# Kernel tuning notes

Hardware: AMD Instinct MI355X
Metric: run time of the kernel (lower is better)

The kernel has to match this reference:

```python
import jax, jax.numpy as jnp
import numpy as np

B, N, IN_DIM, HID = 8, 2048, 128, 64
LN_EPS = 1e-5
NEG_INF = -9e15
LRELU_SLOPE = 0.2


def setup_inputs() -> dict:
    key = jax.random.key(0)
    k1, k2, k3, k4, k5, k6 = jax.random.split(key, 6)
    stdv = 1.0 / np.sqrt(HID)
    adj = jax.random.randint(k1, (B, N, N), 0, 2, dtype=jnp.int32)
    # ensure self-loops so every row has at least one valid entry
    adj = adj.at[:, jnp.arange(N), jnp.arange(N)].set(1)
    return {
        "adj": adj,
        "x": jax.random.normal(k2, (B, N, IN_DIM), dtype=jnp.float32),
        "h": jax.random.normal(k3, (B, N, HID), dtype=jnp.float32),
        "X2H": jax.random.uniform(k4, (IN_DIM, 3 * HID), minval=-stdv, maxval=stdv, dtype=jnp.float32),
        "H2H": jax.random.uniform(k5, (HID, 3 * HID), minval=-stdv, maxval=stdv, dtype=jnp.float32),
        "a": jax.random.uniform(k6, (2 * HID, 1), minval=-stdv, maxval=stdv, dtype=jnp.float32),
    }


def _gated_inputs(x, h, X2H, H2H):
    gate_x = x @ X2H          # [B,N,3H]
    gate_h = h @ H2H          # [B,N,3H]
    i_r, i_i, i_n = jnp.split(gate_x, 3, axis=2)
    h_r, h_i, h_n = jnp.split(gate_h, 3, axis=2)
    resetgate = jax.nn.sigmoid(i_r + h_r)
    inputgate = jax.nn.sigmoid(i_i + h_i)
    irh = i_n + resetgate * h_n
    mu = jnp.mean(irh, axis=-1, keepdims=True)
    var = jnp.mean(jnp.square(irh - mu), axis=-1, keepdims=True)
    irh = (irh - mu) * jax.lax.rsqrt(var + LN_EPS)  # layer_norm, no affine
    newgate = jnp.tanh(irh)
    return newgate + inputgate * (h - newgate)


def reference(adj, x, h, X2H, H2H, a):
    Wh = _gated_inputs(x, h, X2H, H2H)              # [B,N,H]
    Wh1 = Wh @ a[:HID]                              # [B,N,1]
    Wh2 = Wh @ a[HID:]                              # [B,N,1]
    e = jax.nn.leaky_relu(Wh1 + jnp.swapaxes(Wh2, 1, 2), LRELU_SLOPE)  # [B,N,N]
    scores = jnp.where(adj != 0, e, jnp.float32(NEG_INF))
    attention = jax.nn.softmax(scores, axis=2)
    h_prime = attention @ Wh                        # [B,N,H]
    return (h_prime, Wh)
```

## Files before the change

### kernel.cpp

```cpp
#include <hip/hip_runtime.h>

constexpr int BB  = 8;
constexpr int NN  = 2048;
constexpr int IND = 128;
constexpr int HD  = 64;
constexpr float LN_EPS = 1e-5f;
constexpr float SLOPE  = 0.2f;

typedef _Float16 half8 __attribute__((ext_vector_type(8)));
typedef _Float16 half4 __attribute__((ext_vector_type(4)));
typedef float    f32x4 __attribute__((ext_vector_type(4)));

__device__ __forceinline__ float wave_sum(float v) {
    #pragma unroll
    for (int off = 32; off > 0; off >>= 1) v += __shfl_xor(v, off);
    return v;
}
__device__ __forceinline__ float wave_max(float v) {
    #pragma unroll
    for (int off = 32; off > 0; off >>= 1) v = fmaxf(v, __shfl_xor(v, off));
    return v;
}

__global__ void k_prep(const float* __restrict__ X2H, const float* __restrict__ H2H,
                       _Float16* __restrict__ Wt)
{
    const int tot = 256 * 192;
    for (int idx = blockIdx.x * 256 + threadIdx.x; idx < tot; idx += gridDim.x * 256) {
        const int col = idx / 192, k = idx % 192;
        float v;
        if (col < 128)       v = (k < 128) ? X2H[(size_t)k * 192 + col]
                                           : H2H[(size_t)(k - 128) * 192 + col];
        else if (col < 192)  v = (k < 128) ? X2H[(size_t)k * 192 + col] : 0.f;
        else                 v = (k >= 128) ? H2H[(size_t)(k - 128) * 192 + (col - 64)] : 0.f;
        Wt[idx] = (_Float16)v;
    }
}

__global__ __launch_bounds__(256, 4) void k_gates(
    const float* __restrict__ x, const float* __restrict__ h,
    const _Float16* __restrict__ Wt, const float* __restrict__ a,
    float* __restrict__ Wh_out, _Float16* __restrict__ Whh2,
    float* __restrict__ Wh1, float* __restrict__ Wh2)
{
    __shared__ float gbuf[16][260];

    const int tid = threadIdx.x, lane = tid & 63, w = tid >> 6;
    const int m = lane & 15, q = lane >> 4;
    const int row0 = blockIdx.x * 16;

    f32x4 acc[4];
    #pragma unroll
    for (int ct = 0; ct < 4; ++ct) acc[ct] = (f32x4){0.f, 0.f, 0.f, 0.f};

    #pragma unroll
    for (int kc = 0; kc < 6; ++kc) {
        half8 a8;
        if (kc < 4) {
            const float* xp = x + (size_t)(row0 + m) * IND + kc * 32 + q * 8;
            const f32x4 v0 = *(const f32x4*)xp;
            const f32x4 v1 = *(const f32x4*)(xp + 4);
            #pragma unroll
            for (int j = 0; j < 4; ++j) { a8[j] = (_Float16)v0[j]; a8[4 + j] = (_Float16)v1[j]; }
        } else {
            const float* hp_ = h + (size_t)(row0 + m) * HD + (kc - 4) * 32 + q * 8;
            const f32x4 v0 = *(const f32x4*)hp_;
            const f32x4 v1 = *(const f32x4*)(hp_ + 4);
            #pragma unroll
            for (int j = 0; j < 4; ++j) { a8[j] = (_Float16)v0[j]; a8[4 + j] = (_Float16)v1[j]; }
        }
        #pragma unroll
        for (int ct = 0; ct < 4; ++ct) {
            const half8 b8 = *(const half8*)(Wt + ((size_t)(w * 64 + ct * 16 + m) * 192 + kc * 32 + q * 8));
            acc[ct] = __builtin_amdgcn_mfma_f32_16x16x32_f16(a8, b8, acc[ct], 0, 0, 0);
        }
    }

    #pragma unroll
    for (int ct = 0; ct < 4; ++ct)
        #pragma unroll
        for (int r2 = 0; r2 < 4; ++r2)
            gbuf[q * 4 + r2][w * 64 + ct * 16 + m] = acc[ct][r2];
    __syncthreads();

    const float a0 = a[lane], a1 = a[64 + lane];
    half4 p4;
    const int grow0 = row0 + w * 4;
    #pragma unroll
    for (int r = 0; r < 4; ++r) {
        const int row = w * 4 + r;
        const int grow = row0 + row;
        const float g0 = gbuf[row][lane];
        const float g1 = gbuf[row][64 + lane];
        const float g2 = gbuf[row][128 + lane];
        const float g3 = gbuf[row][192 + lane];
        const float rg = 1.f / (1.f + __expf(-g0));
        const float ig = 1.f / (1.f + __expf(-g1));
        const float irh = g2 + rg * g3;
        const float mu = wave_sum(irh) * (1.f / 64.f);
        const float dv = irh - mu;
        const float var = wave_sum(dv * dv) * (1.f / 64.f);
        const float ng = tanhf(dv * rsqrtf(var + LN_EPS));
        const float hr = h[(size_t)grow * HD + lane];
        const float wh = ng + ig * (hr - ng);
        Wh_out[(size_t)grow * HD + lane] = wh;
        p4[r] = (_Float16)wh;
        const float d1 = wave_sum(wh * a0);
        const float d2 = wave_sum(wh * a1);
        if (lane == 0) { Wh1[grow] = d1; Wh2[grow] = d2; }
    }
    *(half4*)(Whh2 + ((size_t)(grow0 >> 3) * 64 + lane) * 8 + (w & 1) * 4) = p4;
}

constexpr int KC  = 256;
constexpr int PST = KC + 8;

__global__ __launch_bounds__(512, 4) void k_attn(
    const int* __restrict__ adj,
    const _Float16* __restrict__ Whh2,
    const float* __restrict__ Wh1, const float* __restrict__ Wh2,
    float* __restrict__ hp)
{
    __shared__ __align__(16) _Float16 Pall[8 * 16 * PST];
    __shared__ float ssum[8][16];
    __shared__ float redb[8];

    const int tid  = threadIdx.x;
    const int lane = tid & 63;
    const int w    = tid >> 6;
    const int b    = blockIdx.x >> 7;
    const int i0   = (blockIdx.x & 127) * 16;
    const int m    = lane & 15;
    const int q    = lane >> 4;

    _Float16* __restrict__ Pw = Pall + w * 16 * PST;

    const f32x4 wv = ((const f32x4*)(Wh2 + (size_t)b * NN))[w * 64 + lane];

    float mx = fmaxf(fmaxf(wv[0], wv[1]), fmaxf(wv[2], wv[3]));
    mx = wave_max(mx);
    if (lane == 0) redb[w] = mx;
    __syncthreads();
    float M = redb[0];
    #pragma unroll
    for (int i = 1; i < 8; ++i) M = fmaxf(M, redb[i]);

    float w1r[16];
    #pragma unroll
    for (int r = 0; r < 16; ++r) w1r[r] = Wh1[b * NN + i0 + r];

    const int* __restrict__ abase = adj + ((size_t)b * NN + i0) * NN + w * KC + 4 * lane;

    int4 buf0[4], buf1[4];
    #pragma unroll
    for (int r = 0; r < 4; ++r) buf0[r] = *(const int4*)(abase + (size_t)r * NN);
    #pragma unroll
    for (int r = 0; r < 4; ++r) buf1[r] = *(const int4*)(abase + (size_t)(4 + r) * NN);

    #pragma unroll
    for (int g = 0; g < 4; ++g) {
        #pragma unroll
        for (int rr = 0; rr < 4; ++rr) {
            const int r = g * 4 + rr;
            const int4 av = (g & 1) ? buf1[rr] : buf0[rr];
            const int ai[4] = {av.x, av.y, av.z, av.w};
            const float t0 = w1r[r] + M;
            const float c  = (t0 > 0.f) ? t0 : SLOPE * t0;
            half4 ph;
            float s = 0.f;
            #pragma unroll
            for (int d = 0; d < 4; ++d) {
                const float t = w1r[r] + wv[d];
                const float e = (t > 0.f) ? t : SLOPE * t;
                const float p = ai[d] ? __expf(e - c) : 0.f;
                s += p;
                ph[d] = (_Float16)p;
            }
            s = wave_sum(s);
            if (lane == 0) ssum[w][r] = s;
            *(half4*)&Pw[r * PST + 4 * lane] = ph;
        }
        if (g + 2 < 4) {
            #pragma unroll
            for (int rr = 0; rr < 4; ++rr) {
                int4 nv = *(const int4*)(abase + (size_t)((g + 2) * 4 + rr) * NN);
                if (g & 1) buf1[rr] = nv; else buf0[rr] = nv;
            }
        }
    }
    __syncthreads();

    const half8* __restrict__ Wp = (const half8*)(Whh2 + (size_t)b * NN * HD);
    f32x4 acc[4];
    #pragma unroll
    for (int cc = 0; cc < 4; ++cc) acc[cc] = (f32x4){0.f, 0.f, 0.f, 0.f};

    #pragma unroll
    for (int k8 = 0; k8 < 8; ++k8) {
        const half8 a8 = *(const half8*)&Pw[m * PST + k8 * 32 + q * 8];
        #pragma unroll
        for (int cc = 0; cc < 4; ++cc) {
            const half8 b8 = Wp[(size_t)(w * 32 + k8 * 4 + q) * 64 + cc * 16 + m];
            acc[cc] = __builtin_amdgcn_mfma_f32_16x16x32_f16(a8, b8, acc[cc], 0, 0, 0);
        }
    }
    __syncthreads();

    float* __restrict__ accb = (float*)Pall;
    #pragma unroll
    for (int cc = 0; cc < 4; ++cc)
        *(f32x4*)&accb[(w * 64 + lane) * 17 + cc * 4] = acc[cc];
    __syncthreads();

    if (w < 4) {
        f32x4 tot = (f32x4){0.f, 0.f, 0.f, 0.f};
        #pragma unroll
        for (int wp = 0; wp < 8; ++wp) {
            const f32x4 t4 = *(const f32x4*)&accb[(wp * 64 + lane) * 17 + w * 4];
            tot[0] += t4[0]; tot[1] += t4[1]; tot[2] += t4[2]; tot[3] += t4[3];
        }
        #pragma unroll
        for (int r2 = 0; r2 < 4; ++r2) {
            const int irow = q * 4 + r2;
            float S = 0.f;
            #pragma unroll
            for (int wp = 0; wp < 8; ++wp) S += ssum[wp][irow];
            hp[((size_t)b * NN + i0 + irow) * HD + w * 16 + m] = tot[r2] / S;
        }
    }
}

extern "C" void kernel_launch(void* const* d_in, const int* in_sizes, int n_in,
                              void* d_out, int out_size, void* d_ws, size_t ws_size,
                              hipStream_t stream) {
    const int*   adj = (const int*)d_in[0];
    const float* x   = (const float*)d_in[1];
    const float* h   = (const float*)d_in[2];
    const float* X2H = (const float*)d_in[3];
    const float* H2H = (const float*)d_in[4];
    const float* a   = (const float*)d_in[5];

    float* out = (float*)d_out;
    float* hp  = out;
    float* Wh  = out + (size_t)BB * NN * HD;

    float*    Wh1  = (float*)d_ws;
    float*    Wh2  = Wh1 + BB * NN;
    _Float16* Whh2 = (_Float16*)(Wh2 + BB * NN);
    _Float16* Wt   = Whh2 + (size_t)BB * NN * HD;

    k_prep<<<dim3(64), dim3(256), 0, stream>>>(X2H, H2H, Wt);
    k_gates<<<dim3((BB * NN) / 16), dim3(256), 0, stream>>>(
        x, h, Wt, a, Wh, Whh2, Wh1, Wh2);
    k_attn<<<dim3(BB * (NN / 16)), dim3(512), 0, stream>>>(
        adj, Whh2, Wh1, Wh2, hp);
}
```

Measured before the change: 239.3 us.

## Factor attention exp into rank-1 terms and compress adjacency into bitmasks

Splits the fused attention kernel into three stages. An aux kernel precomputes per-row and per-column exponential factors, using the fact that leaky-relu of a sum is one of two linear branches, so exp(e - c) factors as u_i*v_j or u'_i*v'_j. A score kernel streams the int32 adjacency once and packs it, together with the branch sign, into 2-bit-per-entry masks. The PV kernel rebuilds P on the fly in fp16 from these factors and computes the row sums with an extra MFMA against ones. This moves the adjacency read into a simple bandwidth-bound pass and removes per-element exp and the LDS round-trip for P. In exchange there are two extra launches, a mask buffer written and re-read, and a possible precision change because the probabilities are now formed as fp16 products.

```diff
diff --git a/kernel.cpp b/kernel.cpp
--- a/kernel.cpp
+++ b/kernel.cpp
@@ -112,122 +112,149 @@
     *(half4*)(Whh2 + ((size_t)(grow0 >> 3) * 64 + lane) * 8 + (w & 1) * 4) = p4;
 }
 
-constexpr int KC  = 256;
-constexpr int PST = KC + 8;
-
-__global__ __launch_bounds__(512, 4) void k_attn(
+__global__ __launch_bounds__(256) void k_aux(
+    const float* __restrict__ Wh1, const float* __restrict__ Wh2,
+    float* __restrict__ u, float* __restrict__ up,
+    _Float16* __restrict__ v16, _Float16* __restrict__ v16p)
+{
+    __shared__ float red[4];
+    const int tid = threadIdx.x, lane = tid & 63, w = tid >> 6;
+    const int b = blockIdx.x >> 3, part = blockIdx.x & 7;
+
+    float mx = -3e38f;
+    #pragma unroll
+    for (int k = 0; k < 8; ++k) mx = fmaxf(mx, Wh2[b * NN + k * 256 + tid]);
+    mx = wave_max(mx);
+    if (lane == 0) red[w] = mx;
+    __syncthreads();
+    const float M = fmaxf(fmaxf(red[0], red[1]), fmaxf(red[2], red[3]));
+
+    const int grow = b * NN + part * 256 + tid;
+    const float t0 = Wh1[grow] + M;
+    const float c  = (t0 > 0.f) ? t0 : SLOPE * t0;
+    u[grow]  = __expf(t0 - c);
+    up[grow] = __expf(SLOPE * t0 - c);
+    const float w2 = Wh2[grow] - M;
+    v16[grow]  = (_Float16)__expf(w2);
+    v16p[grow] = (_Float16)__expf(SLOPE * w2);
+}
+
+__global__ __launch_bounds__(256, 8) void k_score(
     const int* __restrict__ adj,
+    const float* __restrict__ Wh1, const float* __restrict__ Wh2,
+    unsigned short* __restrict__ Mb)
+{
+    const int tid = threadIdx.x;
+    const int4* __restrict__ adj4 = (const int4*)adj;
+
+    #pragma unroll
+    for (int s = 0; s < 4; ++s) {
+        const int row = s * 4096 + blockIdx.x;
+        const int b   = row >> 11;
+        const float negw1 = -Wh1[row];
+
+        const int4 a0 = adj4[(size_t)row * 512 + tid * 2];
+        const int4 a1 = adj4[(size_t)row * 512 + tid * 2 + 1];
+        const f32x4 w0 = ((const f32x4*)(Wh2 + (size_t)b * NN))[tid * 2];
+        const f32x4 w1 = ((const f32x4*)(Wh2 + (size_t)b * NN))[tid * 2 + 1];
+
+        unsigned m1 = 0, m0 = 0;
+        const int av[8] = {a0.x, a0.y, a0.z, a0.w, a1.x, a1.y, a1.z, a1.w};
+        #pragma unroll
+        for (int j = 0; j < 8; ++j) {
+            const float wj = (j < 4) ? w0[j] : w1[j - 4];
+            const bool a = (av[j] != 0);
+            const bool ss = (wj > negw1);
+            m1 |= (unsigned)(a && ss) << j;
+            m0 |= (unsigned)(a && !ss) << j;
+        }
+        Mb[(size_t)row * 256 + tid] = (unsigned short)(m1 | (m0 << 8));
+    }
+}
+
+__global__ __launch_bounds__(256, 4) void k_pv(
+    const unsigned short* __restrict__ Mb,
     const _Float16* __restrict__ Whh2,
-    const float* __restrict__ Wh1, const float* __restrict__ Wh2,
+    const _Float16* __restrict__ v16, const _Float16* __restrict__ v16p,
+    const float* __restrict__ u, const float* __restrict__ up,
     float* __restrict__ hp)
 {
-    __shared__ __align__(16) _Float16 Pall[8 * 16 * PST];
-    __shared__ float ssum[8][16];
-    __shared__ float redb[8];
-
-    const int tid  = threadIdx.x;
-    const int lane = tid & 63;
-    const int w    = tid >> 6;
-    const int b    = blockIdx.x >> 7;
-    const int i0   = (blockIdx.x & 127) * 16;
-    const int m    = lane & 15;
-    const int q    = lane >> 4;
-
-    _Float16* __restrict__ Pw = Pall + w * 16 * PST;
-
-    const f32x4 wv = ((const f32x4*)(Wh2 + (size_t)b * NN))[w * 64 + lane];
-
-    float mx = fmaxf(fmaxf(wv[0], wv[1]), fmaxf(wv[2], wv[3]));
-    mx = wave_max(mx);
-    if (lane == 0) redb[w] = mx;
+    __shared__ float accb[4][64][20];
+    __shared__ float ssumw[4][16];
+
+    const int tid = threadIdx.x, lane = tid & 63, w = tid >> 6;
+    const int m = lane & 15, q = lane >> 4;
+    const int b  = blockIdx.x >> 7;
+    const int i0 = (blockIdx.x & 127) * 16;
+
+    const int grow_m = b * NN + i0 + m;
+    const _Float16 uh  = (_Float16)u[grow_m];
+    const _Float16 uph = (_Float16)up[grow_m];
+
+    const unsigned short* __restrict__ mrow = Mb + (size_t)grow_m * 256 + w * 64;
+    const half8* __restrict__ Wp  = (const half8*)Whh2 + (size_t)b * 16384;
+    const half8* __restrict__ v8  = (const half8*)v16  + b * 256;
+    const half8* __restrict__ v8p = (const half8*)v16p + b * 256;
+
+    half8 ones;
+    #pragma unroll
+    for (int j = 0; j < 8; ++j) ones[j] = (_Float16)1.f;
+
+    f32x4 acc[4];
+    #pragma unroll
+    for (int cc = 0; cc < 4; ++cc) acc[cc] = (f32x4){0.f, 0.f, 0.f, 0.f};
+    f32x4 accS = (f32x4){0.f, 0.f, 0.f, 0.f};
+
+    #pragma unroll
+    for (int k8 = 0; k8 < 16; ++k8) {
+        const int slot  = k8 * 4 + q;
+        const int kpack = w * 64 + slot;
+        const unsigned mb = mrow[slot];
+        const unsigned m1b = mb & 0xFFu, m0b = mb >> 8;
+
+        const half8 vj  = v8[kpack];
+        const half8 vjp = v8p[kpack];
+
+        half8 Ac;
+        #pragma unroll
+        for (int j = 0; j < 8; ++j) {
+            const _Float16 pos = uh * vj[j];
+            const _Float16 neg = uph * vjp[j];
+            Ac[j] = (m1b >> j & 1u) ? pos : ((m0b >> j & 1u) ? neg : (_Float16)0.f);
+        }
+
+        accS = __builtin_amdgcn_mfma_f32_16x16x32_f16(Ac, ones, accS, 0, 0, 0);
+        #pragma unroll
+        for (int cc = 0; cc < 4; ++cc) {
+            const half8 b8 = Wp[(size_t)kpack * 64 + cc * 16 + m];
+            acc[cc] = __builtin_amdgcn_mfma_f32_16x16x32_f16(Ac, b8, acc[cc], 0, 0, 0);
+        }
+    }
+
+    if (m == 0) {
+        #pragma unroll
+        for (int r2 = 0; r2 < 4; ++r2) ssumw[w][q * 4 + r2] = accS[r2];
+    }
+    #pragma unroll
+    for (int cc = 0; cc < 4; ++cc)
+        *(f32x4*)&accb[w][lane][cc * 4] = acc[cc];
     __syncthreads();
-    float M = redb[0];
-    #pragma unroll
-    for (int i = 1; i < 8; ++i) M = fmaxf(M, redb[i]);
-
-    float w1r[16];
-    #pragma unroll
-    for (int r = 0; r < 16; ++r) w1r[r] = Wh1[b * NN + i0 + r];
-
-    const int* __restrict__ abase = adj + ((size_t)b * NN + i0) * NN + w * KC + 4 * lane;
-
-    int4 buf0[4], buf1[4];
-    #pragma unroll
-    for (int r = 0; r < 4; ++r) buf0[r] = *(const int4*)(abase + (size_t)r * NN);
-    #pragma unroll
-    for (int r = 0; r < 4; ++r) buf1[r] = *(const int4*)(abase + (size_t)(4 + r) * NN);
-
-    #pragma unroll
-    for (int g = 0; g < 4; ++g) {
-        #pragma unroll
-        for (int rr = 0; rr < 4; ++rr) {
-            const int r = g * 4 + rr;
-            const int4 av = (g & 1) ? buf1[rr] : buf0[rr];
-            const int ai[4] = {av.x, av.y, av.z, av.w};
-            const float t0 = w1r[r] + M;
-            const float c  = (t0 > 0.f) ? t0 : SLOPE * t0;
-            half4 ph;
-            float s = 0.f;
-            #pragma unroll
-            for (int d = 0; d < 4; ++d) {
-                const float t = w1r[r] + wv[d];
-                const float e = (t > 0.f) ? t : SLOPE * t;
-                const float p = ai[d] ? __expf(e - c) : 0.f;
-                s += p;
-                ph[d] = (_Float16)p;
-            }
-            s = wave_sum(s);
-            if (lane == 0) ssum[w][r] = s;
-            *(half4*)&Pw[r * PST + 4 * lane] = ph;
-        }
-        if (g + 2 < 4) {
-            #pragma unroll
-            for (int rr = 0; rr < 4; ++rr) {
-                int4 nv = *(const int4*)(abase + (size_t)((g + 2) * 4 + rr) * NN);
-                if (g & 1) buf1[rr] = nv; else buf0[rr] = nv;
-            }
-        }
-    }
-    __syncthreads();
-
-    const half8* __restrict__ Wp = (const half8*)(Whh2 + (size_t)b * NN * HD);
-    f32x4 acc[4];
-    #pragma unroll
-    for (int cc = 0; cc < 4; ++cc) acc[cc] = (f32x4){0.f, 0.f, 0.f, 0.f};
-
-    #pragma unroll
-    for (int k8 = 0; k8 < 8; ++k8) {
-        const half8 a8 = *(const half8*)&Pw[m * PST + k8 * 32 + q * 8];
-        #pragma unroll
-        for (int cc = 0; cc < 4; ++cc) {
-            const half8 b8 = Wp[(size_t)(w * 32 + k8 * 4 + q) * 64 + cc * 16 + m];
-            acc[cc] = __builtin_amdgcn_mfma_f32_16x16x32_f16(a8, b8, acc[cc], 0, 0, 0);
-        }
-    }
-    __syncthreads();
-
-    float* __restrict__ accb = (float*)Pall;
-    #pragma unroll
-    for (int cc = 0; cc < 4; ++cc)
-        *(f32x4*)&accb[(w * 64 + lane) * 17 + cc * 4] = acc[cc];
-    __syncthreads();
-
-    if (w < 4) {
-        f32x4 tot = (f32x4){0.f, 0.f, 0.f, 0.f};
-        #pragma unroll
-        for (int wp = 0; wp < 8; ++wp) {
-            const f32x4 t4 = *(const f32x4*)&accb[(wp * 64 + lane) * 17 + w * 4];
-            tot[0] += t4[0]; tot[1] += t4[1]; tot[2] += t4[2]; tot[3] += t4[3];
-        }
-        #pragma unroll
-        for (int r2 = 0; r2 < 4; ++r2) {
-            const int irow = q * 4 + r2;
-            float S = 0.f;
-            #pragma unroll
-            for (int wp = 0; wp < 8; ++wp) S += ssum[wp][irow];
-            hp[((size_t)b * NN + i0 + irow) * HD + w * 16 + m] = tot[r2] / S;
-        }
-    }
+
+    const int row = tid >> 4, c4 = tid & 15;
+    const float S = ssumw[0][row] + ssumw[1][row] + ssumw[2][row] + ssumw[3][row];
+    const int rq = row >> 2, r2 = row & 3;
+    f32x4 tot;
+    #pragma unroll
+    for (int j = 0; j < 4; ++j) {
+        const int col = c4 * 4 + j;
+        const int cc = col >> 4, mm = col & 15;
+        const int ln = rq * 16 + mm;
+        float v = 0.f;
+        #pragma unroll
+        for (int wp = 0; wp < 4; ++wp) v += accb[wp][ln][cc * 4 + r2];
+        tot[j] = v / S;
+    }
+    *(f32x4*)(hp + ((size_t)(b * NN + i0 + row)) * HD + c4 * 4) = tot;
 }
 
 extern "C" void kernel_launch(void* const* d_in, const int* in_sizes, int n_in,
@@ -246,12 +273,19 @@
 
     float*    Wh1  = (float*)d_ws;
     float*    Wh2  = Wh1 + BB * NN;
-    _Float16* Whh2 = (_Float16*)(Wh2 + BB * NN);
+    float*    u    = Wh2 + BB * NN;
+    float*    up   = u + BB * NN;
+    _Float16* v16  = (_Float16*)(up + BB * NN);
+    _Float16* v16p = v16 + BB * NN;
+    _Float16* Whh2 = v16p + BB * NN;
     _Float16* Wt   = Whh2 + (size_t)BB * NN * HD;
+    unsigned short* Mb = (unsigned short*)(Wt + 256 * 192);
 
     k_prep<<<dim3(64), dim3(256), 0, stream>>>(X2H, H2H, Wt);
     k_gates<<<dim3((BB * NN) / 16), dim3(256), 0, stream>>>(
         x, h, Wt, a, Wh, Whh2, Wh1, Wh2);
-    k_attn<<<dim3(BB * (NN / 16)), dim3(512), 0, stream>>>(
-        adj, Whh2, Wh1, Wh2, hp);
-}
+    k_aux<<<dim3(64), dim3(256), 0, stream>>>(Wh1, Wh2, u, up, v16, v16p);
+    k_score<<<dim3(4096), dim3(256), 0, stream>>>(adj, Wh1, Wh2, Mb);
+    k_pv<<<dim3(BB * (NN / 16)), dim3(256), 0, stream>>>(
+        Mb, Whh2, v16, v16p, u, up, hp);
+}
```

Result: slower. 256.9 us (+7.4%).
